# Kernel tuning notes

Hardware: AMD Instinct MI355X
Metric: run time of the kernel (lower is better)

## Reference

```python
import jax, jax.numpy as jnp
import numpy as np

N, E, D_IN, D_H, D_OUT = 50000, 640000, 128, 128, 64
EPS = 1e-5


def _sage(x, src, dst, Wl, bl, Wr):
    # PyG SAGEConv: out = lin_l(mean_{j in N(i)} x_j) + lin_r(x_i)
    msg = x[src]                                             # [E, d] gather
    agg = jax.ops.segment_sum(msg, dst, num_segments=x.shape[0])
    deg = jax.ops.segment_sum(jnp.ones((src.shape[0],), x.dtype), dst,
                              num_segments=x.shape[0])
    agg = agg / jnp.maximum(deg, 1.0)[:, None]               # mean aggregate
    return agg @ Wl + bl + x @ Wr


def _bn_eval(x, gamma, beta, mean, var):
    return (x - mean) * jax.lax.rsqrt(var + EPS) * gamma + beta


def setup_inputs() -> dict:
    key = jax.random.key(0)
    ks = jax.random.split(key, 16)
    s = lambda d: 1.0 / np.sqrt(d)
    inp = {
        "x": jax.random.normal(ks[0], (N, D_IN), jnp.float32),
        "edge_index": jax.random.randint(ks[1], (2, E), 0, N, jnp.int64),
        # layer 0: 128 -> 128
        "Wl0": jax.random.normal(ks[2], (D_IN, D_H), jnp.float32) * s(D_IN),
        "bl0": jnp.zeros((D_H,), jnp.float32),
        "Wr0": jax.random.normal(ks[3], (D_IN, D_H), jnp.float32) * s(D_IN),
        # layer 1: 128 -> 128
        "Wl1": jax.random.normal(ks[4], (D_H, D_H), jnp.float32) * s(D_H),
        "bl1": jnp.zeros((D_H,), jnp.float32),
        "Wr1": jax.random.normal(ks[5], (D_H, D_H), jnp.float32) * s(D_H),
        # layer 2: 128 -> 64
        "Wl2": jax.random.normal(ks[6], (D_H, D_OUT), jnp.float32) * s(D_H),
        "bl2": jnp.zeros((D_OUT,), jnp.float32),
        "Wr2": jax.random.normal(ks[7], (D_H, D_OUT), jnp.float32) * s(D_H),
        # BatchNorm (eval mode) for the two hidden layers
        "g0": jnp.ones((D_H,), jnp.float32),
        "b0": jnp.zeros((D_H,), jnp.float32),
        "m0": jax.random.normal(ks[8], (D_H,), jnp.float32) * 0.1,
        "v0": jax.random.uniform(ks[9], (D_H,), jnp.float32, 0.5, 1.5),
        "g1": jnp.ones((D_H,), jnp.float32),
        "b1": jnp.zeros((D_H,), jnp.float32),
        "m1": jax.random.normal(ks[10], (D_H,), jnp.float32) * 0.1,
        "v1": jax.random.uniform(ks[11], (D_H,), jnp.float32, 0.5, 1.5),
    }
    return inp


def reference(x, edge_index, Wl0, bl0, Wr0, Wl1, bl1, Wr1, Wl2, bl2, Wr2,
              g0, b0, m0, v0, g1, b1, m1, v1):
    src, dst = edge_index[0], edge_index[1]
    # edge mask (edge_index < N) is all-true by construction -> no-op
    h = _sage(x, src, dst, Wl0, bl0, Wr0)
    h = jax.nn.relu(_bn_eval(h, g0, b0, m0, v0))   # eval: dropout is identity
    h = _sage(h, src, dst, Wl1, bl1, Wr1)
    h = jax.nn.relu(_bn_eval(h, g1, b1, m1, v1))
    h = _sage(h, src, dst, Wl2, bl2, Wr2)
    return jax.nn.log_softmax(h, axis=1)
```

## Files before the change

kernel.cpp:

```cpp
#include <hip/hip_runtime.h>

#define EPS 1e-5f
#define ELL_CAP 64
#define BLK 256
#define BUILD_BLOCKS 128
#define CTP 136

typedef __attribute__((ext_vector_type(8))) short short8;
typedef __attribute__((ext_vector_type(4))) float f32x4;
typedef __attribute__((ext_vector_type(2))) float f32x2;

__device__ inline unsigned short f2b(float f) {
    union { float f; unsigned u; } v; v.f = f;
    unsigned u = v.u;
    return (unsigned short)((u + 0x7fffu + ((u >> 16) & 1u)) >> 16);
}
__device__ inline float b2f(unsigned short u) {
    union { unsigned u; float f; } v;
    v.u = ((unsigned)u) << 16;
    return v.f;
}


__device__ inline void cvt_one(const float* Wl, const float* Wr,
                               unsigned short* BT, int dout, int idx) {
    int n = idx >> 7, k = idx & 127;
    float w = (n < dout) ? Wl[k * dout + n] : Wr[k * dout + (n - dout)];
    BT[idx] = f2b(w);
}

__global__ void k_prep(const float* __restrict__ Wl0, const float* __restrict__ Wr0,
                       const float* __restrict__ Wl1, const float* __restrict__ Wr1,
                       const float* __restrict__ Wl2, const float* __restrict__ Wr2,
                       unsigned short* __restrict__ BT0,
                       unsigned short* __restrict__ BT1,
                       unsigned short* __restrict__ BT2,
                       int* __restrict__ cnt, int N) {
    int idx = blockIdx.x * blockDim.x + threadIdx.x;
    if (idx < N) cnt[idx] = 0;
    const int S0 = 256 * 128, S1 = 256 * 128, S2 = 128 * 128;
    if (idx < S0) cvt_one(Wl0, Wr0, BT0, 128, idx);
    else if (idx < S0 + S1) cvt_one(Wl1, Wr1, BT1, 128, idx - S0);
    else if (idx < S0 + S1 + S2) cvt_one(Wl2, Wr2, BT2, 64, idx - S0 - S1);
}


__device__ inline short8 pack8(float4 a, float4 b) {
    short8 r;
    r[0] = (short)f2b(a.x); r[1] = (short)f2b(a.y);
    r[2] = (short)f2b(a.z); r[3] = (short)f2b(a.w);
    r[4] = (short)f2b(b.x); r[5] = (short)f2b(b.y);
    r[6] = (short)f2b(b.z); r[7] = (short)f2b(b.w);
    return r;
}

template <int NCOLS, bool A32, int OUT>
__device__ inline void gemm_tile(unsigned short* Bs,
                                 const void* __restrict__ Av,
                                 const unsigned short* __restrict__ BT,
                                 unsigned short* __restrict__ C,
                                 unsigned char* __restrict__ P8,
                                 unsigned short* __restrict__ Qb,
                                 int M, int bx, int by) {
    const int tid  = threadIdx.x;
    const int lane = tid & 63;
    const int wave = tid >> 6;
    const int m16  = lane & 15;
    const int q    = lane >> 4;
    const int row0 = (bx * 4 + wave) * 16;
    const int col0 = by * 128;

#pragma unroll
    for (int i = 0; i < 8; ++i) {
        int f   = tid + i * 256;
        int t   = f >> 8;
        int kc  = (f >> 6) & 3;
        int ln  = f & 63;
        int bm  = ln & 15, bq = ln >> 4;
        const short8* gp = (const short8*)(BT + (size_t)(col0 + t * 16 + bm) * 128
                                              + kc * 32 + bq * 8);
        *(short8*)(Bs + (size_t)f * 8) = *gp;
    }

    int arow = row0 + m16;
    if (arow >= M) arow = M - 1;
    short8 af0, af1, af2, af3;
    if (A32) {
        const float4* Ap = (const float4*)((const float*)Av + (size_t)arow * 128 + q * 8);
        af0 = pack8(Ap[0],  Ap[1]);
        af1 = pack8(Ap[8],  Ap[9]);
        af2 = pack8(Ap[16], Ap[17]);
        af3 = pack8(Ap[24], Ap[25]);
    } else {
        const short8* Ap = (const short8*)((const unsigned short*)Av + (size_t)arow * 128 + q * 8);
        af0 = Ap[0]; af1 = Ap[4]; af2 = Ap[8]; af3 = Ap[12];
    }

    __syncthreads();

    f32x4 acc[8] = {};
#pragma unroll
    for (int t = 0; t < 8; ++t) {
        const short8* bp = (const short8*)(Bs + (size_t)(t * 4) * 64 * 8 + (size_t)lane * 8);
        short8 b0 = bp[0];
        short8 b1 = bp[64];
        short8 b2 = bp[128];
        short8 b3 = bp[192];
        acc[t] = __builtin_amdgcn_mfma_f32_16x16x32_bf16(af0, b0, acc[t], 0, 0, 0);
        acc[t] = __builtin_amdgcn_mfma_f32_16x16x32_bf16(af1, b1, acc[t], 0, 0, 0);
        acc[t] = __builtin_amdgcn_mfma_f32_16x16x32_bf16(af2, b2, acc[t], 0, 0, 0);
        acc[t] = __builtin_amdgcn_mfma_f32_16x16x32_bf16(af3, b3, acc[t], 0, 0, 0);
    }

    __syncthreads();
#pragma unroll
    for (int t = 0; t < 8; ++t)
#pragma unroll
        for (int r = 0; r < 4; ++r)
            Bs[(wave * 16 + q * 4 + r) * CTP + t * 16 + m16] = f2b(acc[t][r]);
    __syncthreads();

    const int rowBase = bx * 64;
    for (int f = tid; f < 16 * 64; f += BLK) {
        int row = f >> 4, c8 = f & 15;
        int grow = rowBase + row;
        if (grow >= M) continue;
        short8 vv = *(short8*)(Bs + row * CTP + c8 * 8);
        if (OUT == 0) {
            *(short8*)(C + (size_t)grow * NCOLS + col0 + c8 * 8) = vv;
        } else if (by == 1) {
            *(short8*)(Qb + (size_t)grow * 128 + c8 * 8) = vv;
        } else {
            int lo = __builtin_amdgcn_cvt_pk_fp8_f32(
                b2f((unsigned short)vv[0]), b2f((unsigned short)vv[1]), 0, false);
            lo = __builtin_amdgcn_cvt_pk_fp8_f32(
                b2f((unsigned short)vv[2]), b2f((unsigned short)vv[3]), lo, true);
            int hi = __builtin_amdgcn_cvt_pk_fp8_f32(
                b2f((unsigned short)vv[4]), b2f((unsigned short)vv[5]), 0, false);
            hi = __builtin_amdgcn_cvt_pk_fp8_f32(
                b2f((unsigned short)vv[6]), b2f((unsigned short)vv[7]), hi, true);
            uint2 st; st.x = (unsigned)lo; st.y = (unsigned)hi;
            *(uint2*)(P8 + (size_t)grow * 128 + c8 * 8) = st;
        }
    }
    __syncthreads();
}


__global__ void k_mega(const int* __restrict__ src, const int* __restrict__ dst,
                       int E, int* __restrict__ cnt, unsigned short* __restrict__ ell,
                       const float* __restrict__ x,
                       const unsigned short* __restrict__ BT0,
                       unsigned char* __restrict__ P8,
                       unsigned short* __restrict__ Qb, int M) {
    __shared__ __align__(16) unsigned short Bs[8 * 4 * 64 * 8];

    if ((int)blockIdx.x < BUILD_BLOCKS) {
        const int T = BUILD_BLOCKS * BLK;
        int i = blockIdx.x * BLK + threadIdx.x;
        for (int base = 0; base < E; base += 4 * T) {
            int e0 = base + i, e1 = e0 + T, e2 = e1 + T, e3 = e2 + T;
            int d0 = 0, d1 = 0, d2 = 0, d3 = 0;
            int s0 = 0, s1 = 0, s2 = 0, s3 = 0;
            if (e0 < E) { d0 = dst[e0]; s0 = src[e0]; }
            if (e1 < E) { d1 = dst[e1]; s1 = src[e1]; }
            if (e2 < E) { d2 = dst[e2]; s2 = src[e2]; }
            if (e3 < E) { d3 = dst[e3]; s3 = src[e3]; }
            int p0 = 0, p1 = 0, p2 = 0, p3 = 0;
            if (e0 < E) p0 = atomicAdd(&cnt[d0], 1);
            if (e1 < E) p1 = atomicAdd(&cnt[d1], 1);
            if (e2 < E) p2 = atomicAdd(&cnt[d2], 1);
            if (e3 < E) p3 = atomicAdd(&cnt[d3], 1);
            if (e0 < E && p0 < ELL_CAP) ell[(size_t)d0 * ELL_CAP + p0] = (unsigned short)s0;
            if (e1 < E && p1 < ELL_CAP) ell[(size_t)d1 * ELL_CAP + p1] = (unsigned short)s1;
            if (e2 < E && p2 < ELL_CAP) ell[(size_t)d2 * ELL_CAP + p2] = (unsigned short)s2;
            if (e3 < E && p3 < ELL_CAP) ell[(size_t)d3 * ELL_CAP + p3] = (unsigned short)s3;
        }
        return;
    }
    int bid = blockIdx.x - BUILD_BLOCKS;
    gemm_tile<256, true, 1>(Bs, x, BT0, nullptr, P8, Qb, M, bid >> 1, bid & 1);
}


__global__ void k_gemm1(const unsigned short* __restrict__ A,
                        const unsigned short* __restrict__ BT,
                        unsigned char* __restrict__ P8,
                        unsigned short* __restrict__ Qb, int M) {
    __shared__ __align__(16) unsigned short Bs[8 * 4 * 64 * 8];
    gemm_tile<256, false, 1>(Bs, A, BT, nullptr, P8, Qb, M, blockIdx.x, blockIdx.y);
}

__global__ void k_gemm2(const unsigned short* __restrict__ A,
                        const unsigned short* __restrict__ BT,
                        unsigned short* __restrict__ C, int M) {
    __shared__ __align__(16) unsigned short Bs[8 * 4 * 64 * 8];
    gemm_tile<128, false, 0>(Bs, A, BT, C, nullptr, nullptr, M, blockIdx.x, 0);
}


__global__ void k_agg128(const unsigned char* __restrict__ P8,
                         const unsigned short* __restrict__ Qb,
                         const int* __restrict__ cnt,
                         const unsigned short* __restrict__ ell,
                         const float* __restrict__ bl,
                         const float* __restrict__ g, const float* __restrict__ b,
                         const float* __restrict__ m, const float* __restrict__ v,
                         unsigned short* __restrict__ out, int n) {
    int node = (blockIdx.x * blockDim.x + threadIdx.x) >> 6;
    int lane = threadIdx.x & 63;
    if (node >= n) return;
    int cn  = cnt[node];
    int deg = min(cn, ELL_CAP);
    int myidx = (lane < deg) ? (int)ell[(size_t)node * ELL_CAP + lane] : 0;
    const int half = lane >> 5, hl = lane & 31;

    float a0 = 0.f, a1 = 0.f, a2 = 0.f, a3 = 0.f;
    int j = 0;
    for (; j + 4 <= deg; j += 4) {
        int ia = __shfl(myidx, j + half);
        int ib = __shfl(myidx, j + 2 + half);
        unsigned wa = *(const unsigned*)(P8 + (size_t)ia * 128 + 4 * hl);
        unsigned wb = *(const unsigned*)(P8 + (size_t)ib * 128 + 4 * hl);
        f32x2 la = __builtin_amdgcn_cvt_pk_f32_fp8(wa, false);
        f32x2 ha = __builtin_amdgcn_cvt_pk_f32_fp8(wa, true);
        f32x2 lb = __builtin_amdgcn_cvt_pk_f32_fp8(wb, false);
        f32x2 hb2 = __builtin_amdgcn_cvt_pk_f32_fp8(wb, true);
        a0 += la[0] + lb[0];
        a1 += la[1] + lb[1];
        a2 += ha[0] + hb2[0];
        a3 += ha[1] + hb2[1];
    }
    for (; j < deg; j += 2) {
        int rem = deg - j;
        int ia = __shfl(myidx, min(j + half, deg - 1));
        if (half == 0 || rem >= 2) {
            unsigned wa = *(const unsigned*)(P8 + (size_t)ia * 128 + 4 * hl);
            f32x2 la = __builtin_amdgcn_cvt_pk_f32_fp8(wa, false);
            f32x2 ha = __builtin_amdgcn_cvt_pk_f32_fp8(wa, true);
            a0 += la[0]; a1 += la[1]; a2 += ha[0]; a3 += ha[1];
        }
    }
    a0 += __shfl_xor(a0, 32);
    a1 += __shfl_xor(a1, 32);
    a2 += __shfl_xor(a2, 32);
    a3 += __shfl_xor(a3, 32);

    float dg = fmaxf((float)cn, 1.f);
    ushort4 qv = *(const ushort4*)(Qb + (size_t)node * 128 + 4 * hl);
    int c0 = 4 * hl;
    float4 blv = *(const float4*)(bl + c0);
    float4 mv  = *(const float4*)(m + c0);
    float4 vv  = *(const float4*)(v + c0);
    float4 gv  = *(const float4*)(g + c0);
    float4 bv  = *(const float4*)(b + c0);
    float z0 = (a0 / dg + b2f(qv.x) + blv.x - mv.x) * rsqrtf(vv.x + EPS) * gv.x + bv.x;
    float z1 = (a1 / dg + b2f(qv.y) + blv.y - mv.y) * rsqrtf(vv.y + EPS) * gv.y + bv.y;
    float z2 = (a2 / dg + b2f(qv.z) + blv.z - mv.z) * rsqrtf(vv.z + EPS) * gv.z + bv.z;
    float z3 = (a3 / dg + b2f(qv.w) + blv.w - mv.w) * rsqrtf(vv.w + EPS) * gv.w + bv.w;
    if (half == 0) {
        ushort4 r;
        r.x = f2b(fmaxf(z0, 0.f));
        r.y = f2b(fmaxf(z1, 0.f));
        r.z = f2b(fmaxf(z2, 0.f));
        r.w = f2b(fmaxf(z3, 0.f));
        *(ushort4*)(out + (size_t)node * 128 + c0) = r;
    }
}


__global__ void k_agg64(const unsigned short* __restrict__ PQ,
                        const int* __restrict__ cnt,
                        const unsigned short* __restrict__ ell,
                        const float* __restrict__ bl,
                        float* __restrict__ out, int n) {
    int node = (blockIdx.x * blockDim.x + threadIdx.x) >> 6;
    int lane = threadIdx.x & 63;
    if (node >= n) return;
    int cn  = cnt[node];
    int deg = min(cn, ELL_CAP);
    int myidx = (lane < deg) ? (int)ell[(size_t)node * ELL_CAP + lane] : 0;
    const int qtr = lane >> 4, ql = lane & 15;

    float a0 = 0.f, a1 = 0.f, a2 = 0.f, a3 = 0.f;
    int j = 0;
    for (; j + 8 <= deg; j += 8) {
        int ia = __shfl(myidx, j + qtr);
        int ib = __shfl(myidx, j + 4 + qtr);
        ushort4 pa = *(const ushort4*)(PQ + (size_t)ia * 128 + 4 * ql);
        ushort4 pb = *(const ushort4*)(PQ + (size_t)ib * 128 + 4 * ql);
        a0 += b2f(pa.x) + b2f(pb.x);
        a1 += b2f(pa.y) + b2f(pb.y);
        a2 += b2f(pa.z) + b2f(pb.z);
        a3 += b2f(pa.w) + b2f(pb.w);
    }
    for (; j < deg; j += 4) {
        int rem = deg - j;
        int ia = __shfl(myidx, min(j + qtr, deg - 1));
        if (qtr < rem) {
            ushort4 pa = *(const ushort4*)(PQ + (size_t)ia * 128 + 4 * ql);
            a0 += b2f(pa.x); a1 += b2f(pa.y); a2 += b2f(pa.z); a3 += b2f(pa.w);
        }
    }
    a0 += __shfl_xor(a0, 16); a0 += __shfl_xor(a0, 32);
    a1 += __shfl_xor(a1, 16); a1 += __shfl_xor(a1, 32);
    a2 += __shfl_xor(a2, 16); a2 += __shfl_xor(a2, 32);
    a3 += __shfl_xor(a3, 16); a3 += __shfl_xor(a3, 32);

    float dg = fmaxf((float)cn, 1.f);
    ushort4 qv = *(const ushort4*)(PQ + (size_t)node * 128 + 64 + 4 * ql);
    int c0 = 4 * ql;
    float4 blv = *(const float4*)(bl + c0);
    float z0 = a0 / dg + b2f(qv.x) + blv.x;
    float z1 = a1 / dg + b2f(qv.y) + blv.y;
    float z2 = a2 / dg + b2f(qv.z) + blv.z;
    float z3 = a3 / dg + b2f(qv.w) + blv.w;

    float mx = fmaxf(fmaxf(z0, z1), fmaxf(z2, z3));
#pragma unroll
    for (int off = 8; off > 0; off >>= 1) mx = fmaxf(mx, __shfl_xor(mx, off));
    float sm = __expf(z0 - mx) + __expf(z1 - mx) + __expf(z2 - mx) + __expf(z3 - mx);
#pragma unroll
    for (int off = 8; off > 0; off >>= 1) sm += __shfl_xor(sm, off);
    float lg = mx + __logf(sm);
    if (qtr == 0) {
        float4 o = make_float4(z0 - lg, z1 - lg, z2 - lg, z3 - lg);
        *(float4*)(out + (size_t)node * 64 + c0) = o;
    }
}


extern "C" void kernel_launch(void* const* d_in, const int* in_sizes, int n_in,
                              void* d_out, int out_size, void* d_ws, size_t ws_size,
                              hipStream_t stream) {
    const float* x   = (const float*)d_in[0];
    const int*   ei  = (const int*)d_in[1];
    const float* Wl0 = (const float*)d_in[2];
    const float* bl0 = (const float*)d_in[3];
    const float* Wr0 = (const float*)d_in[4];
    const float* Wl1 = (const float*)d_in[5];
    const float* bl1 = (const float*)d_in[6];
    const float* Wr1 = (const float*)d_in[7];
    const float* Wl2 = (const float*)d_in[8];
    const float* bl2 = (const float*)d_in[9];
    const float* Wr2 = (const float*)d_in[10];
    const float* g0  = (const float*)d_in[11];
    const float* b0  = (const float*)d_in[12];
    const float* m0  = (const float*)d_in[13];
    const float* v0  = (const float*)d_in[14];
    const float* g1  = (const float*)d_in[15];
    const float* b1  = (const float*)d_in[16];
    const float* m1  = (const float*)d_in[17];
    const float* v1  = (const float*)d_in[18];

    const int N = in_sizes[0] / 128;
    const int E = in_sizes[1] / 2;
    const int* src = ei;
    const int* dst = ei + E;

    size_t off = 0;
    auto alloc = [&](size_t bytes) -> void* {
        void* p = (char*)d_ws + off;
        off += (bytes + 255) & ~(size_t)255;
        return p;
    };
    int* cnt = (int*)alloc((size_t)N * 4);
    unsigned short* ell = (unsigned short*)alloc((size_t)N * ELL_CAP * 2);
    unsigned char*  P8  = (unsigned char*)alloc((size_t)N * 128);
    unsigned short* Qb  = (unsigned short*)alloc((size_t)N * 128 * 2);
    unsigned short* PQ  = (unsigned short*)alloc((size_t)N * 128 * 2);
    unsigned short* hb  = (unsigned short*)alloc((size_t)N * 128 * 2);
    unsigned short* BT0 = (unsigned short*)alloc((size_t)256 * 128 * 2);
    unsigned short* BT1 = (unsigned short*)alloc((size_t)256 * 128 * 2);
    unsigned short* BT2 = (unsigned short*)alloc((size_t)128 * 128 * 2);
    (void)ws_size;

    const int CVT_TOTAL = 256 * 128 + 256 * 128 + 128 * 128;
    int prepGrid = (max(CVT_TOTAL, N) + BLK - 1) / BLK;
    k_prep<<<prepGrid, BLK, 0, stream>>>(Wl0, Wr0, Wl1, Wr1, Wl2, Wr2,
                                         BT0, BT1, BT2, cnt, N);

    int rowBlocks = (N + 63) / 64;
    dim3 mg2(rowBlocks, 2);
    int aggGrid = (N + 3) / 4;

    int gemmBlocks = rowBlocks * 2;
    k_mega<<<BUILD_BLOCKS + gemmBlocks, BLK, 0, stream>>>(
        src, dst, E, cnt, ell, x, BT0, P8, Qb, N);

    k_agg128<<<aggGrid, BLK, 0, stream>>>(P8, Qb, cnt, ell, bl0, g0, b0, m0, v0, hb, N);
    k_gemm1<<<mg2, BLK, 0, stream>>>(hb, BT1, P8, Qb, N);
    k_agg128<<<aggGrid, BLK, 0, stream>>>(P8, Qb, cnt, ell, bl1, g1, b1, m1, v1, hb, N);
    k_gemm2<<<rowBlocks, BLK, 0, stream>>>(hb, BT2, PQ, N);
    k_agg64<<<aggGrid, BLK, 0, stream>>>(PQ, cnt, ell, bl2, (float*)d_out, N);
}
```

Measured before the change: 250.5 us.

## Fuse neighbor aggregation with following layer GEMM via shared-memory tile

Merges each mid-layer aggregation kernel with the next layer's GEMM. A block of four waves first aggregates 64 nodes, writing the normalized ReLU rows into a shared-memory tile. It then runs the MFMA GEMM directly from that tile, so the hidden activation never goes to global memory and two launches disappear. Because the fused kernel reads the previous layer's projections while writing new ones, it needs ping-pong P8/Qb buffers. In exchange, each wave now walks 16 nodes serially, giving far fewer blocks and less latency hiding for the irregular gather, and the extra LDS lowers occupancy.

```diff
diff --git a/kernel.cpp b/kernel.cpp
--- a/kernel.cpp
+++ b/kernel.cpp
@@ -54,22 +54,8 @@
     return r;
 }
 
-template <int NCOLS, bool A32, int OUT>
-__device__ inline void gemm_tile(unsigned short* Bs,
-                                 const void* __restrict__ Av,
-                                 const unsigned short* __restrict__ BT,
-                                 unsigned short* __restrict__ C,
-                                 unsigned char* __restrict__ P8,
-                                 unsigned short* __restrict__ Qb,
-                                 int M, int bx, int by) {
-    const int tid  = threadIdx.x;
-    const int lane = tid & 63;
-    const int wave = tid >> 6;
-    const int m16  = lane & 15;
-    const int q    = lane >> 4;
-    const int row0 = (bx * 4 + wave) * 16;
-    const int col0 = by * 128;
-
+__device__ inline void stage_B(unsigned short* Bs, const unsigned short* __restrict__ BT,
+                               int col0, int tid) {
 #pragma unroll
     for (int i = 0; i < 8; ++i) {
         int f   = tid + i * 256;
@@ -81,24 +67,10 @@
                                               + kc * 32 + bq * 8);
         *(short8*)(Bs + (size_t)f * 8) = *gp;
     }
-
-    int arow = row0 + m16;
-    if (arow >= M) arow = M - 1;
-    short8 af0, af1, af2, af3;
-    if (A32) {
-        const float4* Ap = (const float4*)((const float*)Av + (size_t)arow * 128 + q * 8);
-        af0 = pack8(Ap[0],  Ap[1]);
-        af1 = pack8(Ap[8],  Ap[9]);
-        af2 = pack8(Ap[16], Ap[17]);
-        af3 = pack8(Ap[24], Ap[25]);
-    } else {
-        const short8* Ap = (const short8*)((const unsigned short*)Av + (size_t)arow * 128 + q * 8);
-        af0 = Ap[0]; af1 = Ap[4]; af2 = Ap[8]; af3 = Ap[12];
-    }
-
-    __syncthreads();
-
-    f32x4 acc[8] = {};
+}
+
+__device__ inline void mfma_8t(f32x4* acc, const unsigned short* Bs, int lane,
+                               short8 af0, short8 af1, short8 af2, short8 af3) {
 #pragma unroll
     for (int t = 0; t < 8; ++t) {
         const short8* bp = (const short8*)(Bs + (size_t)(t * 4) * 64 * 8 + (size_t)lane * 8);
@@ -111,7 +83,15 @@
         acc[t] = __builtin_amdgcn_mfma_f32_16x16x32_bf16(af2, b2, acc[t], 0, 0, 0);
         acc[t] = __builtin_amdgcn_mfma_f32_16x16x32_bf16(af3, b3, acc[t], 0, 0, 0);
     }
-
+}
+
+template <int MODE, int NC>
+__device__ inline void epilogue(unsigned short* Bs, const f32x4* acc,
+                                unsigned short* __restrict__ Cb,
+                                unsigned char* __restrict__ C8,
+                                int M, int rowBase, int colOff,
+                                int tid, int lane, int wave) {
+    const int m16 = lane & 15, q = lane >> 4;
     __syncthreads();
 #pragma unroll
     for (int t = 0; t < 8; ++t)
@@ -119,17 +99,13 @@
         for (int r = 0; r < 4; ++r)
             Bs[(wave * 16 + q * 4 + r) * CTP + t * 16 + m16] = f2b(acc[t][r]);
     __syncthreads();
-
-    const int rowBase = bx * 64;
     for (int f = tid; f < 16 * 64; f += BLK) {
         int row = f >> 4, c8 = f & 15;
         int grow = rowBase + row;
         if (grow >= M) continue;
         short8 vv = *(short8*)(Bs + row * CTP + c8 * 8);
-        if (OUT == 0) {
-            *(short8*)(C + (size_t)grow * NCOLS + col0 + c8 * 8) = vv;
-        } else if (by == 1) {
-            *(short8*)(Qb + (size_t)grow * 128 + c8 * 8) = vv;
+        if (MODE == 0) {
+            *(short8*)(Cb + (size_t)grow * NC + colOff + c8 * 8) = vv;
         } else {
             int lo = __builtin_amdgcn_cvt_pk_fp8_f32(
                 b2f((unsigned short)vv[0]), b2f((unsigned short)vv[1]), 0, false);
@@ -140,10 +116,78 @@
             hi = __builtin_amdgcn_cvt_pk_fp8_f32(
                 b2f((unsigned short)vv[6]), b2f((unsigned short)vv[7]), hi, true);
             uint2 st; st.x = (unsigned)lo; st.y = (unsigned)hi;
-            *(uint2*)(P8 + (size_t)grow * 128 + c8 * 8) = st;
+            *(uint2*)(C8 + (size_t)grow * 128 + c8 * 8) = st;
         }
     }
     __syncthreads();
+}
+
+
+__device__ inline void agg128_core(const unsigned char* __restrict__ P8,
+                                   const unsigned short* __restrict__ Qb,
+                                   const int* __restrict__ cnt,
+                                   const unsigned short* __restrict__ ell,
+                                   const float* __restrict__ bl,
+                                   const float* __restrict__ g, const float* __restrict__ b,
+                                   const float* __restrict__ m, const float* __restrict__ v,
+                                   unsigned short* __restrict__ dstRow,
+                                   int node, int lane) {
+    int cn  = cnt[node];
+    int deg = min(cn, ELL_CAP);
+    int myidx = (lane < deg) ? (int)ell[(size_t)node * ELL_CAP + lane] : 0;
+    const int half = lane >> 5, hl = lane & 31;
+
+    float a0 = 0.f, a1 = 0.f, a2 = 0.f, a3 = 0.f;
+    int j = 0;
+    for (; j + 4 <= deg; j += 4) {
+        int ia = __shfl(myidx, j + half);
+        int ib = __shfl(myidx, j + 2 + half);
+        unsigned wa = *(const unsigned*)(P8 + (size_t)ia * 128 + 4 * hl);
+        unsigned wb = *(const unsigned*)(P8 + (size_t)ib * 128 + 4 * hl);
+        f32x2 la = __builtin_amdgcn_cvt_pk_f32_fp8(wa, false);
+        f32x2 ha = __builtin_amdgcn_cvt_pk_f32_fp8(wa, true);
+        f32x2 lb = __builtin_amdgcn_cvt_pk_f32_fp8(wb, false);
+        f32x2 hb2 = __builtin_amdgcn_cvt_pk_f32_fp8(wb, true);
+        a0 += la[0] + lb[0];
+        a1 += la[1] + lb[1];
+        a2 += ha[0] + hb2[0];
+        a3 += ha[1] + hb2[1];
+    }
+    for (; j < deg; j += 2) {
+        int rem = deg - j;
+        int ia = __shfl(myidx, min(j + half, deg - 1));
+        if (half == 0 || rem >= 2) {
+            unsigned wa = *(const unsigned*)(P8 + (size_t)ia * 128 + 4 * hl);
+            f32x2 la = __builtin_amdgcn_cvt_pk_f32_fp8(wa, false);
+            f32x2 ha = __builtin_amdgcn_cvt_pk_f32_fp8(wa, true);
+            a0 += la[0]; a1 += la[1]; a2 += ha[0]; a3 += ha[1];
+        }
+    }
+    a0 += __shfl_xor(a0, 32);
+    a1 += __shfl_xor(a1, 32);
+    a2 += __shfl_xor(a2, 32);
+    a3 += __shfl_xor(a3, 32);
+
+    float dg = fmaxf((float)cn, 1.f);
+    ushort4 qv = *(const ushort4*)(Qb + (size_t)node * 128 + 4 * hl);
+    int c0 = 4 * hl;
+    float4 blv = *(const float4*)(bl + c0);
+    float4 mv  = *(const float4*)(m + c0);
+    float4 vv  = *(const float4*)(v + c0);
+    float4 gv  = *(const float4*)(g + c0);
+    float4 bv  = *(const float4*)(b + c0);
+    float z0 = (a0 / dg + b2f(qv.x) + blv.x - mv.x) * rsqrtf(vv.x + EPS) * gv.x + bv.x;
+    float z1 = (a1 / dg + b2f(qv.y) + blv.y - mv.y) * rsqrtf(vv.y + EPS) * gv.y + bv.y;
+    float z2 = (a2 / dg + b2f(qv.z) + blv.z - mv.z) * rsqrtf(vv.z + EPS) * gv.z + bv.z;
+    float z3 = (a3 / dg + b2f(qv.w) + blv.w - mv.w) * rsqrtf(vv.w + EPS) * gv.w + bv.w;
+    if (half == 0) {
+        ushort4 r;
+        r.x = f2b(fmaxf(z0, 0.f));
+        r.y = f2b(fmaxf(z1, 0.f));
+        r.z = f2b(fmaxf(z2, 0.f));
+        r.w = f2b(fmaxf(z3, 0.f));
+        *(ushort4*)(dstRow + c0) = r;
+    }
 }
 
 
@@ -179,92 +223,85 @@
         return;
     }
     int bid = blockIdx.x - BUILD_BLOCKS;
-    gemm_tile<256, true, 1>(Bs, x, BT0, nullptr, P8, Qb, M, bid >> 1, bid & 1);
-}
-
-
-__global__ void k_gemm1(const unsigned short* __restrict__ A,
-                        const unsigned short* __restrict__ BT,
-                        unsigned char* __restrict__ P8,
-                        unsigned short* __restrict__ Qb, int M) {
+    int bx = bid >> 1, by = bid & 1;
+    const int tid  = threadIdx.x;
+    const int lane = tid & 63;
+    const int wave = tid >> 6;
+    const int m16  = lane & 15;
+    const int q    = lane >> 4;
+    const int row0 = (bx * 4 + wave) * 16;
+
+    stage_B(Bs, BT0, by * 128, tid);
+
+    int arow = row0 + m16;
+    if (arow >= M) arow = M - 1;
+    const float4* Ap = (const float4*)(x + (size_t)arow * 128 + q * 8);
+    short8 af0 = pack8(Ap[0],  Ap[1]);
+    short8 af1 = pack8(Ap[8],  Ap[9]);
+    short8 af2 = pack8(Ap[16], Ap[17]);
+    short8 af3 = pack8(Ap[24], Ap[25]);
+
+    __syncthreads();
+    f32x4 acc[8] = {};
+    mfma_8t(acc, Bs, lane, af0, af1, af2, af3);
+
+    if (by == 0) epilogue<1, 128>(Bs, acc, nullptr, P8, M, bx * 64, 0, tid, lane, wave);
+    else         epilogue<0, 128>(Bs, acc, Qb, nullptr, M, bx * 64, 0, tid, lane, wave);
+}
+
+
+template <int OUTK>
+__global__ void k_fuse(const unsigned char* __restrict__ P8in,
+                       const unsigned short* __restrict__ Qbin,
+                       const int* __restrict__ cnt,
+                       const unsigned short* __restrict__ ell,
+                       const float* __restrict__ bl,
+                       const float* __restrict__ g, const float* __restrict__ b,
+                       const float* __restrict__ m, const float* __restrict__ v,
+                       const unsigned short* __restrict__ BT,
+                       unsigned char* __restrict__ P8out,
+                       unsigned short* __restrict__ Qbout,
+                       unsigned short* __restrict__ Cout,
+                       int N) {
     __shared__ __align__(16) unsigned short Bs[8 * 4 * 64 * 8];
-    gemm_tile<256, false, 1>(Bs, A, BT, nullptr, P8, Qb, M, blockIdx.x, blockIdx.y);
-}
-
-__global__ void k_gemm2(const unsigned short* __restrict__ A,
-                        const unsigned short* __restrict__ BT,
-                        unsigned short* __restrict__ C, int M) {
-    __shared__ __align__(16) unsigned short Bs[8 * 4 * 64 * 8];
-    gemm_tile<128, false, 0>(Bs, A, BT, C, nullptr, nullptr, M, blockIdx.x, 0);
-}
-
-
-__global__ void k_agg128(const unsigned char* __restrict__ P8,
-                         const unsigned short* __restrict__ Qb,
-                         const int* __restrict__ cnt,
-                         const unsigned short* __restrict__ ell,
-                         const float* __restrict__ bl,
-                         const float* __restrict__ g, const float* __restrict__ b,
-                         const float* __restrict__ m, const float* __restrict__ v,
-                         unsigned short* __restrict__ out, int n) {
-    int node = (blockIdx.x * blockDim.x + threadIdx.x) >> 6;
-    int lane = threadIdx.x & 63;
-    if (node >= n) return;
-    int cn  = cnt[node];
-    int deg = min(cn, ELL_CAP);
-    int myidx = (lane < deg) ? (int)ell[(size_t)node * ELL_CAP + lane] : 0;
-    const int half = lane >> 5, hl = lane & 31;
-
-    float a0 = 0.f, a1 = 0.f, a2 = 0.f, a3 = 0.f;
-    int j = 0;
-    for (; j + 4 <= deg; j += 4) {
-        int ia = __shfl(myidx, j + half);
-        int ib = __shfl(myidx, j + 2 + half);
-        unsigned wa = *(const unsigned*)(P8 + (size_t)ia * 128 + 4 * hl);
-        unsigned wb = *(const unsigned*)(P8 + (size_t)ib * 128 + 4 * hl);
-        f32x2 la = __builtin_amdgcn_cvt_pk_f32_fp8(wa, false);
-        f32x2 ha = __builtin_amdgcn_cvt_pk_f32_fp8(wa, true);
-        f32x2 lb = __builtin_amdgcn_cvt_pk_f32_fp8(wb, false);
-        f32x2 hb2 = __builtin_amdgcn_cvt_pk_f32_fp8(wb, true);
-        a0 += la[0] + lb[0];
-        a1 += la[1] + lb[1];
-        a2 += ha[0] + hb2[0];
-        a3 += ha[1] + hb2[1];
-    }
-    for (; j < deg; j += 2) {
-        int rem = deg - j;
-        int ia = __shfl(myidx, min(j + half, deg - 1));
-        if (half == 0 || rem >= 2) {
-            unsigned wa = *(const unsigned*)(P8 + (size_t)ia * 128 + 4 * hl);
-            f32x2 la = __builtin_amdgcn_cvt_pk_f32_fp8(wa, false);
-            f32x2 ha = __builtin_amdgcn_cvt_pk_f32_fp8(wa, true);
-            a0 += la[0]; a1 += la[1]; a2 += ha[0]; a3 += ha[1];
-        }
-    }
-    a0 += __shfl_xor(a0, 32);
-    a1 += __shfl_xor(a1, 32);
-    a2 += __shfl_xor(a2, 32);
-    a3 += __shfl_xor(a3, 32);
-
-    float dg = fmaxf((float)cn, 1.f);
-    ushort4 qv = *(const ushort4*)(Qb + (size_t)node * 128 + 4 * hl);
-    int c0 = 4 * hl;
-    float4 blv = *(const float4*)(bl + c0);
-    float4 mv  = *(const float4*)(m + c0);
-    float4 vv  = *(const float4*)(v + c0);
-    float4 gv  = *(const float4*)(g + c0);
-    float4 bv  = *(const float4*)(b + c0);
-    float z0 = (a0 / dg + b2f(qv.x) + blv.x - mv.x) * rsqrtf(vv.x + EPS) * gv.x + bv.x;
-    float z1 = (a1 / dg + b2f(qv.y) + blv.y - mv.y) * rsqrtf(vv.y + EPS) * gv.y + bv.y;
-    float z2 = (a2 / dg + b2f(qv.z) + blv.z - mv.z) * rsqrtf(vv.z + EPS) * gv.z + bv.z;
-    float z3 = (a3 / dg + b2f(qv.w) + blv.w - mv.w) * rsqrtf(vv.w + EPS) * gv.w + bv.w;
-    if (half == 0) {
-        ushort4 r;
-        r.x = f2b(fmaxf(z0, 0.f));
-        r.y = f2b(fmaxf(z1, 0.f));
-        r.z = f2b(fmaxf(z2, 0.f));
-        r.w = f2b(fmaxf(z3, 0.f));
-        *(ushort4*)(out + (size_t)node * 128 + c0) = r;
+    __shared__ __align__(16) unsigned short Ht[64 * CTP];
+
+    const int tid  = threadIdx.x;
+    const int lane = tid & 63;
+    const int wave = tid >> 6;
+    const int m16  = lane & 15;
+    const int q    = lane >> 4;
+    const int baseNode = blockIdx.x * 64;
+
+    for (int k = 0; k < 16; ++k) {
+        int lrow = wave * 16 + k;
+        int node = baseNode + lrow;
+        if (node < N)
+            agg128_core(P8in, Qbin, cnt, ell, bl, g, b, m, v,
+                        Ht + (size_t)lrow * CTP, node, lane);
+    }
+    __syncthreads();
+
+    const unsigned short* ar = Ht + (size_t)(wave * 16 + m16) * CTP + q * 8;
+    short8 af0 = *(const short8*)(ar);
+    short8 af1 = *(const short8*)(ar + 32);
+    short8 af2 = *(const short8*)(ar + 64);
+    short8 af3 = *(const short8*)(ar + 96);
+
+    stage_B(Bs, BT, 0, tid);
+    __syncthreads();
+    {
+        f32x4 acc[8] = {};
+        mfma_8t(acc, Bs, lane, af0, af1, af2, af3);
+        if (OUTK == 1) epilogue<1, 128>(Bs, acc, nullptr, P8out, N, baseNode, 0, tid, lane, wave);
+        else           epilogue<0, 128>(Bs, acc, Cout, nullptr, N, baseNode, 0, tid, lane, wave);
+    }
+    if (OUTK == 1) {
+        stage_B(Bs, BT, 128, tid);
+        __syncthreads();
+        f32x4 acc[8] = {};
+        mfma_8t(acc, Bs, lane, af0, af1, af2, af3);
+        epilogue<0, 128>(Bs, acc, Qbout, nullptr, N, baseNode, 0, tid, lane, wave);
     }
 }
 
@@ -365,14 +402,15 @@
         return p;
     };
     int* cnt = (int*)alloc((size_t)N * 4);
-    unsigned short* ell = (unsigned short*)alloc((size_t)N * ELL_CAP * 2);
-    unsigned char*  P8  = (unsigned char*)alloc((size_t)N * 128);
-    unsigned short* Qb  = (unsigned short*)alloc((size_t)N * 128 * 2);
-    unsigned short* PQ  = (unsigned short*)alloc((size_t)N * 128 * 2);
-    unsigned short* hb  = (unsigned short*)alloc((size_t)N * 128 * 2);
-    unsigned short* BT0 = (unsigned short*)alloc((size_t)256 * 128 * 2);
-    unsigned short* BT1 = (unsigned short*)alloc((size_t)256 * 128 * 2);
-    unsigned short* BT2 = (unsigned short*)alloc((size_t)128 * 128 * 2);
+    unsigned short* ell  = (unsigned short*)alloc((size_t)N * ELL_CAP * 2);
+    unsigned char*  P8a  = (unsigned char*)alloc((size_t)N * 128);
+    unsigned short* Qba  = (unsigned short*)alloc((size_t)N * 128 * 2);
+    unsigned char*  P8b  = (unsigned char*)alloc((size_t)N * 128);
+    unsigned short* Qbb  = (unsigned short*)alloc((size_t)N * 128 * 2);
+    unsigned short* PQ   = (unsigned short*)alloc((size_t)N * 128 * 2);
+    unsigned short* BT0  = (unsigned short*)alloc((size_t)256 * 128 * 2);
+    unsigned short* BT1  = (unsigned short*)alloc((size_t)256 * 128 * 2);
+    unsigned short* BT2  = (unsigned short*)alloc((size_t)128 * 128 * 2);
     (void)ws_size;
 
     const int CVT_TOTAL = 256 * 128 + 256 * 128 + 128 * 128;
@@ -381,16 +419,16 @@
                                          BT0, BT1, BT2, cnt, N);
 
     int rowBlocks = (N + 63) / 64;
-    dim3 mg2(rowBlocks, 2);
     int aggGrid = (N + 3) / 4;
 
-    int gemmBlocks = rowBlocks * 2;
-    k_mega<<<BUILD_BLOCKS + gemmBlocks, BLK, 0, stream>>>(
-        src, dst, E, cnt, ell, x, BT0, P8, Qb, N);
-
-    k_agg128<<<aggGrid, BLK, 0, stream>>>(P8, Qb, cnt, ell, bl0, g0, b0, m0, v0, hb, N);
-    k_gemm1<<<mg2, BLK, 0, stream>>>(hb, BT1, P8, Qb, N);
-    k_agg128<<<aggGrid, BLK, 0, stream>>>(P8, Qb, cnt, ell, bl1, g1, b1, m1, v1, hb, N);
-    k_gemm2<<<rowBlocks, BLK, 0, stream>>>(hb, BT2, PQ, N);
+    k_mega<<<BUILD_BLOCKS + rowBlocks * 2, BLK, 0, stream>>>(
+        src, dst, E, cnt, ell, x, BT0, P8a, Qba, N);
+
+    k_fuse<1><<<rowBlocks, BLK, 0, stream>>>(P8a, Qba, cnt, ell,
+                                             bl0, g0, b0, m0, v0,
+                                             BT1, P8b, Qbb, nullptr, N);
+    k_fuse<0><<<rowBlocks, BLK, 0, stream>>>(P8b, Qbb, cnt, ell,
+                                             bl1, g1, b1, m1, v1,
+                                             BT2, nullptr, nullptr, PQ, N);
     k_agg64<<<aggGrid, BLK, 0, stream>>>(PQ, cnt, ell, bl2, (float*)d_out, N);
 }
```

New measurement: 350.3 us. +39.8%, slower.
